# Optimization experiments

Hardware: AMD Instinct MI355X
Metric: run time of the kernel (lower is better)

Reference implementation:

```python
import jax, jax.numpy as jnp
import numpy as np

TOP_K = 10
RANKING_WEIGHT = 0.3
UP_WEIGHT = 1.0
DOWN_WEIGHT = 0.5
NEG = 1e9  # finite stand-in for -inf so softmax/grads stay NaN-free


def setup_inputs() -> dict:
    key = jax.random.key(0)
    k1, k2, k3, k4 = jax.random.split(key, 4)
    B, N = 1024, 5000
    up_logits = jax.random.normal(k1, (B, N), jnp.float32)
    down_logits = jax.random.normal(k2, (B, N), jnp.float32)
    y_true = jax.random.normal(k3, (B, N), jnp.float32) * 0.05  # daily returns
    masks = jax.random.randint(k4, (B, N), 0, 2).astype(jnp.int32)
    return {"up_logits": up_logits, "down_logits": down_logits,
            "y_true": y_true, "masks": masks}


def _bce_with_logits(x, z):
    # softplus(x) - x*z  ==  -[z*log(sig(x)) + (1-z)*log(1-sig(x))]
    return jax.nn.softplus(x) - x * z


def reference(up_logits, down_logits, y_true, masks):
    maskb = masks > 0                                   # [B, N]
    maskf = maskb.astype(up_logits.dtype)
    num_valid = maskf.sum(-1)                           # [B]
    nv_safe = jnp.maximum(num_valid, 1.0)
    k = jnp.minimum(TOP_K, num_valid.astype(jnp.int32))  # [B] min(top_k, num)

    # Descending rank of y_true among valid entries (invalid pushed to bottom).
    y_desc = jnp.where(maskb, y_true, -NEG)
    rank_desc = jnp.argsort(jnp.argsort(-y_desc, axis=-1), axis=-1)  # [B, N]
    up_labels = (rank_desc < k[:, None]).astype(up_logits.dtype)

    # Ascending rank (biggest losers) for down path.
    y_asc = jnp.where(maskb, y_true, NEG)
    rank_asc = jnp.argsort(jnp.argsort(y_asc, axis=-1), axis=-1)
    down_labels = (rank_asc < k[:, None]).astype(down_logits.dtype)

    # Mean BCE over valid entries per row.
    up_loss = jnp.sum(_bce_with_logits(up_logits, up_labels) * maskf, -1) / nv_safe
    down_loss = jnp.sum(_bce_with_logits(down_logits, down_labels) * maskf, -1) / nv_safe

    # Listwise KL: softmax over valid entries; kl_div(log p, q, 'batchmean')
    # with 1D input of size num divides the sum by num.
    logp = jax.nn.log_softmax(jnp.where(maskb, up_logits, -NEG), axis=-1)
    logq = jax.nn.log_softmax(jnp.where(maskb, y_true, -NEG), axis=-1)
    q = jnp.exp(logq)
    kl = jnp.sum(jnp.where(maskb, q * (logq - logp), 0.0), -1) / nv_safe

    batch_loss = UP_WEIGHT * up_loss + DOWN_WEIGHT * down_loss + RANKING_WEIGHT * kl
    batch_loss = jnp.where(num_valid > 0, batch_loss, 0.0)  # skip empty rows
    return jnp.sum(batch_loss) / up_logits.shape[0]
```

## Files before the change

### kernel.cpp

```cpp
#include <hip/hip_runtime.h>
#include <math.h>

#define NCOLS 5000
#define NF4   1250
#define BLOCK 256
#define NITER 5
#define TOPKK 10

__device__ __forceinline__ unsigned mono_f32(float f) {
  unsigned u = __float_as_uint(f);
  return (u & 0x80000000u) ? ~u : (u | 0x80000000u);
}

__device__ __forceinline__ float wave_sum_f(float v) {
#pragma unroll
  for (int o = 1; o < 64; o <<= 1) v += __shfl_xor(v, o);
  return v;
}
__device__ __forceinline__ int wave_sum_i(int v) {
#pragma unroll
  for (int o = 1; o < 64; o <<= 1) v += __shfl_xor(v, o);
  return v;
}
__device__ __forceinline__ unsigned wave_max_u(unsigned v) {
#pragma unroll
  for (int o = 1; o < 64; o <<= 1) {
    unsigned w = __shfl_xor(v, o);
    v = w > v ? w : v;
  }
  return v;
}

__device__ __forceinline__ void insert_desc(unsigned* L, unsigned key) {
  if (key > L[TOPKK - 1]) {
    L[TOPKK - 1] = key;
#pragma unroll
    for (int p = TOPKK - 1; p > 0; --p) {
      unsigned a = L[p - 1], b = L[p];
      L[p - 1] = b > a ? b : a;
      L[p]     = b > a ? a : b;
    }
  }
}

extern "C" __global__ __launch_bounds__(BLOCK, 4)
void row_loss_kernel(const float* __restrict__ up, const float* __restrict__ down,
                     const float* __restrict__ yt, const int* __restrict__ masks,
                     float* __restrict__ out, float inv_nrows) {
  __shared__ float red_f[6][4];
  __shared__ int red_i[4];
  __shared__ unsigned swtop[4 * TOPKK];
  __shared__ unsigned swbot[4 * TOPKK];
  __shared__ unsigned s_thr[2];
  __shared__ float red2[2][4];

  const int row = blockIdx.x;
  const int tid = threadIdx.x;
  const int lane = tid & 63;
  const int wv = tid >> 6;
  const long long b4 = (long long)row * NF4;

  const float4* up4 = (const float4*)up + b4;
  const float4* dn4 = (const float4*)down + b4;
  const float4* yt4 = (const float4*)yt + b4;
  const int4*   mk4 = (const int4*)masks + b4;

  float ym[NITER][4], uu[NITER][4], dd[NITER][4];

  int nv_l = 0;
  float sq = 0.f, sp = 0.f, seyy = 0.f, seyu = 0.f, aspu = 0.f, aspd = 0.f;
  unsigned td[TOPKK], ta[TOPKK];
#pragma unroll
  for (int j = 0; j < TOPKK; ++j) { td[j] = 0u; ta[j] = 0u; }

#pragma unroll
  for (int j = 0; j < NITER; ++j) {
    const int f = j * BLOCK + tid;
    const bool inb = (f < NF4);
    float4 y4 = make_float4(0.f, 0.f, 0.f, 0.f);
    float4 u4 = y4, d4 = y4;
    int4 m4 = make_int4(0, 0, 0, 0);
    if (inb) { y4 = yt4[f]; u4 = up4[f]; d4 = dn4[f]; m4 = mk4[f]; }
    const float* yp = (const float*)&y4;
    const float* upp = (const float*)&u4;
    const float* dp = (const float*)&d4;
    const int* mp = (const int*)&m4;
#pragma unroll
    for (int c = 0; c < 4; ++c) {
      const bool valid = mp[c] > 0;
      const float y = yp[c], u = upp[c], d = dp[c];
      ym[j][c] = valid ? y : -1e9f;
      uu[j][c] = u;
      dd[j][c] = d;
      if (valid) {
        nv_l++;
        const float ey = __expf(y);
        sq += ey;
        seyy += ey * y;
        seyu += ey * u;
        sp += __expf(u);
        aspu += fmaxf(u, 0.f) + __logf(1.f + __expf(-fabsf(u)));
        aspd += fmaxf(d, 0.f) + __logf(1.f + __expf(-fabsf(d)));
        const unsigned kd = mono_f32(y);
        insert_desc(td, kd);
        insert_desc(ta, ~kd);
      }
    }
  }

  nv_l = wave_sum_i(nv_l);
  sq = wave_sum_f(sq);
  sp = wave_sum_f(sp);
  seyy = wave_sum_f(seyy);
  seyu = wave_sum_f(seyu);
  aspu = wave_sum_f(aspu);
  aspd = wave_sum_f(aspd);
  if (lane == 0) {
    red_i[wv] = nv_l;
    red_f[0][wv] = sq;  red_f[1][wv] = sp;
    red_f[2][wv] = seyy; red_f[3][wv] = seyu;
    red_f[4][wv] = aspu; red_f[5][wv] = aspd;
  }

#pragma unroll 1
  for (int r = 0; r < TOPKK; ++r) {
    unsigned m = wave_max_u(td[0]);
    if (td[0] == m && m != 0u) {
#pragma unroll
      for (int j = 0; j < TOPKK - 1; ++j) td[j] = td[j + 1];
      td[TOPKK - 1] = 0u;
    }
    if (lane == 0) swtop[wv * TOPKK + r] = m;
  }
#pragma unroll 1
  for (int r = 0; r < TOPKK; ++r) {
    unsigned m = wave_max_u(ta[0]);
    if (ta[0] == m && m != 0u) {
#pragma unroll
      for (int j = 0; j < TOPKK - 1; ++j) ta[j] = ta[j + 1];
      ta[TOPKK - 1] = 0u;
    }
    if (lane == 0) swbot[wv * TOPKK + r] = m;
  }
  __syncthreads();

  const int nv = red_i[0] + red_i[1] + red_i[2] + red_i[3];
  const int k = nv < TOPKK ? nv : TOPKK;

  if (wv == 0) {
    unsigned v = (lane < 4 * TOPKK) ? swtop[lane] : 0u;
    unsigned thr = 0xFFFFFFFFu;
#pragma unroll 1
    for (int r = 0; r < TOPKK; ++r) {
      unsigned m = wave_max_u(v);
      if (v == m) v = 0u;
      if (r == k - 1) thr = m;
    }
    if (lane == 0) s_thr[0] = thr;
  } else if (wv == 1) {
    unsigned v = (lane < 4 * TOPKK) ? swbot[lane] : 0u;
    unsigned thr = 0xFFFFFFFFu;
#pragma unroll 1
    for (int r = 0; r < TOPKK; ++r) {
      unsigned m = wave_max_u(v);
      if (v == m) v = 0u;
      if (r == k - 1) thr = m;
    }
    if (lane == 0) s_thr[1] = thr;
  }
  __syncthreads();

  const unsigned thr_top = s_thr[0];
  const unsigned thr_bot = s_thr[1];

  float su = 0.f, sd = 0.f;
#pragma unroll
  for (int j = 0; j < NITER; ++j) {
#pragma unroll
    for (int c = 0; c < 4; ++c) {
      const float y = ym[j][c];
      if (y > -1e8f) {
        const unsigned mo = mono_f32(y);
        if (mo >= thr_top) su += uu[j][c];
        if (~mo >= thr_bot) sd += dd[j][c];
      }
    }
  }
  su = wave_sum_f(su);
  sd = wave_sum_f(sd);
  if (lane == 0) { red2[0][wv] = su; red2[1][wv] = sd; }
  __syncthreads();

  if (tid == 0 && nv > 0) {
    const float SQ = (red_f[0][0] + red_f[0][1]) + (red_f[0][2] + red_f[0][3]);
    const float SP = (red_f[1][0] + red_f[1][1]) + (red_f[1][2] + red_f[1][3]);
    const float SYY = (red_f[2][0] + red_f[2][1]) + (red_f[2][2] + red_f[2][3]);
    const float SYU = (red_f[3][0] + red_f[3][1]) + (red_f[3][2] + red_f[3][3]);
    const float ASU = (red_f[4][0] + red_f[4][1]) + (red_f[4][2] + red_f[4][3]);
    const float ASD = (red_f[5][0] + red_f[5][1]) + (red_f[5][2] + red_f[5][3]);
    const float SU = (red2[0][0] + red2[0][1]) + (red2[0][2] + red2[0][3]);
    const float SD = (red2[1][0] + red2[1][1]) + (red2[1][2] + red2[1][3]);
    const float kl = (SYY - SYU) / SQ - __logf(SQ) + __logf(SP);
    const float up_loss = ASU - SU;
    const float dn_loss = ASD - SD;
    const float loss = (up_loss + 0.5f * dn_loss + 0.3f * kl) / (float)nv;
    atomicAdd(out, loss * inv_nrows);
  }
}

extern "C" void kernel_launch(void* const* d_in, const int* in_sizes, int n_in,
                              void* d_out, int out_size, void* d_ws, size_t ws_size,
                              hipStream_t stream) {
  const float* up_logits   = (const float*)d_in[0];
  const float* down_logits = (const float*)d_in[1];
  const float* y_true      = (const float*)d_in[2];
  const int*   masks       = (const int*)d_in[3];

  const int nrows = in_sizes[0] / NCOLS;

  hipMemsetAsync(d_out, 0, sizeof(float) * (size_t)out_size, stream);
  row_loss_kernel<<<nrows, BLOCK, 0, stream>>>(up_logits, down_logits, y_true,
                                               masks, (float*)d_out,
                                               1.0f / (float)nrows);
}
```

Before: 126.1 us.

## Replace per-thread top-k insertion with shared-memory radix histogram selection

Replaces the per-thread sorted top-10 lists and wave-level merges with a 256-bin shared histogram on the top byte of each key. Prefix scans over the histogram locate the bin holding the k-th largest and k-th smallest keys, then only keys in those bins are gathered and refined with wave max/min. The block size doubles to 512 threads, all loads are issued before compute, and the register-heavy insertion sorts go away. The cost is shared-memory atomic contention on a histogram that may be skewed, plus more barriers. The gather caps a boundary bin at 64 keys, which could give wrong thresholds if more keys share that top byte.

```diff
diff --git a/kernel.cpp b/kernel.cpp
--- a/kernel.cpp
+++ b/kernel.cpp
@@ -3,8 +3,9 @@
 
 #define NCOLS 5000
 #define NF4   1250
-#define BLOCK 256
-#define NITER 5
+#define BLOCK 512
+#define NWAVES (BLOCK / 64)
+#define NITER 3
 #define TOPKK 10
 
 __device__ __forceinline__ unsigned mono_f32(float f) {
@@ -30,29 +31,27 @@
   }
   return v;
 }
-
-__device__ __forceinline__ void insert_desc(unsigned* L, unsigned key) {
-  if (key > L[TOPKK - 1]) {
-    L[TOPKK - 1] = key;
-#pragma unroll
-    for (int p = TOPKK - 1; p > 0; --p) {
-      unsigned a = L[p - 1], b = L[p];
-      L[p - 1] = b > a ? b : a;
-      L[p]     = b > a ? a : b;
-    }
-  }
+__device__ __forceinline__ unsigned wave_min_u(unsigned v) {
+#pragma unroll
+  for (int o = 1; o < 64; o <<= 1) {
+    unsigned w = __shfl_xor(v, o);
+    v = w < v ? w : v;
+  }
+  return v;
 }
 
 extern "C" __global__ __launch_bounds__(BLOCK, 4)
 void row_loss_kernel(const float* __restrict__ up, const float* __restrict__ down,
                      const float* __restrict__ yt, const int* __restrict__ masks,
                      float* __restrict__ out, float inv_nrows) {
-  __shared__ float red_f[6][4];
-  __shared__ int red_i[4];
-  __shared__ unsigned swtop[4 * TOPKK];
-  __shared__ unsigned swbot[4 * TOPKK];
+  __shared__ unsigned hist[256];
+  __shared__ float red_f[6][NWAVES];
+  __shared__ int red_i[NWAVES];
+  __shared__ unsigned s_sel[4];
   __shared__ unsigned s_thr[2];
-  __shared__ float red2[2][4];
+  __shared__ unsigned keys_t[64], keys_b[64];
+  __shared__ int cnt_t, cnt_b;
+  __shared__ float red2[2][NWAVES];
 
   const int row = blockIdx.x;
   const int tid = threadIdx.x;
@@ -65,26 +64,33 @@
   const float4* yt4 = (const float4*)yt + b4;
   const int4*   mk4 = (const int4*)masks + b4;
 
+  float4 y4[NITER], u4[NITER], d4[NITER];
+  int4 m4[NITER];
+#pragma unroll
+  for (int j = 0; j < NITER; ++j) {
+    const int f = j * BLOCK + tid;
+    if (f < NF4) {
+      y4[j] = yt4[f]; u4[j] = up4[f]; d4[j] = dn4[f]; m4[j] = mk4[f];
+    } else {
+      y4[j] = make_float4(0.f, 0.f, 0.f, 0.f);
+      u4[j] = y4[j]; d4[j] = y4[j];
+      m4[j] = make_int4(0, 0, 0, 0);
+    }
+  }
+
+  if (tid < 256) hist[tid] = 0u;
+  if (tid == 0) { cnt_t = 0; cnt_b = 0; }
+  __syncthreads();
+
   float ym[NITER][4], uu[NITER][4], dd[NITER][4];
-
   int nv_l = 0;
   float sq = 0.f, sp = 0.f, seyy = 0.f, seyu = 0.f, aspu = 0.f, aspd = 0.f;
-  unsigned td[TOPKK], ta[TOPKK];
-#pragma unroll
-  for (int j = 0; j < TOPKK; ++j) { td[j] = 0u; ta[j] = 0u; }
-
-#pragma unroll
-  for (int j = 0; j < NITER; ++j) {
-    const int f = j * BLOCK + tid;
-    const bool inb = (f < NF4);
-    float4 y4 = make_float4(0.f, 0.f, 0.f, 0.f);
-    float4 u4 = y4, d4 = y4;
-    int4 m4 = make_int4(0, 0, 0, 0);
-    if (inb) { y4 = yt4[f]; u4 = up4[f]; d4 = dn4[f]; m4 = mk4[f]; }
-    const float* yp = (const float*)&y4;
-    const float* upp = (const float*)&u4;
-    const float* dp = (const float*)&d4;
-    const int* mp = (const int*)&m4;
+#pragma unroll
+  for (int j = 0; j < NITER; ++j) {
+    const float* yp = (const float*)&y4[j];
+    const float* upp = (const float*)&u4[j];
+    const float* dp = (const float*)&d4[j];
+    const int* mp = (const int*)&m4[j];
 #pragma unroll
     for (int c = 0; c < 4; ++c) {
       const bool valid = mp[c] > 0;
@@ -101,9 +107,7 @@
         sp += __expf(u);
         aspu += fmaxf(u, 0.f) + __logf(1.f + __expf(-fabsf(u)));
         aspd += fmaxf(d, 0.f) + __logf(1.f + __expf(-fabsf(d)));
-        const unsigned kd = mono_f32(y);
-        insert_desc(td, kd);
-        insert_desc(ta, ~kd);
+        atomicAdd(&hist[mono_f32(y) >> 24], 1u);
       }
     }
   }
@@ -121,68 +125,128 @@
     red_f[2][wv] = seyy; red_f[3][wv] = seyu;
     red_f[4][wv] = aspu; red_f[5][wv] = aspd;
   }
-
-#pragma unroll 1
-  for (int r = 0; r < TOPKK; ++r) {
-    unsigned m = wave_max_u(td[0]);
-    if (td[0] == m && m != 0u) {
-#pragma unroll
-      for (int j = 0; j < TOPKK - 1; ++j) td[j] = td[j + 1];
-      td[TOPKK - 1] = 0u;
-    }
-    if (lane == 0) swtop[wv * TOPKK + r] = m;
-  }
-#pragma unroll 1
-  for (int r = 0; r < TOPKK; ++r) {
-    unsigned m = wave_max_u(ta[0]);
-    if (ta[0] == m && m != 0u) {
-#pragma unroll
-      for (int j = 0; j < TOPKK - 1; ++j) ta[j] = ta[j + 1];
-      ta[TOPKK - 1] = 0u;
-    }
-    if (lane == 0) swbot[wv * TOPKK + r] = m;
-  }
-  __syncthreads();
-
-  const int nv = red_i[0] + red_i[1] + red_i[2] + red_i[3];
+  __syncthreads();
+
+  int nv = 0;
+#pragma unroll
+  for (int w = 0; w < NWAVES; ++w) nv += red_i[w];
   const int k = nv < TOPKK ? nv : TOPKK;
 
   if (wv == 0) {
-    unsigned v = (lane < 4 * TOPKK) ? swtop[lane] : 0u;
-    unsigned thr = 0xFFFFFFFFu;
-#pragma unroll 1
-    for (int r = 0; r < TOPKK; ++r) {
-      unsigned m = wave_max_u(v);
-      if (v == m) v = 0u;
-      if (r == k - 1) thr = m;
-    }
-    if (lane == 0) s_thr[0] = thr;
+    unsigned h[4];
+#pragma unroll
+    for (int j = 0; j < 4; ++j) h[j] = hist[4 * lane + j];
+    const unsigned s = h[0] + h[1] + h[2] + h[3];
+    unsigned suf = s;
+#pragma unroll
+    for (int o = 1; o < 64; o <<= 1) {
+      int src = lane + o;
+      unsigned g = __shfl(suf, src < 64 ? src : lane);
+      suf += (src < 64) ? g : 0u;
+    }
+    unsigned long long mb = __ballot(suf >= (unsigned)k);
+    if (mb != 0ULL) {
+      int lstar = 63 - __builtin_clzll(mb);
+      if (lane == lstar) {
+        unsigned cum = suf - s;
+        int bin = -1; unsigned cab = 0;
+#pragma unroll
+        for (int j = 3; j >= 0; --j) {
+          unsigned nc = cum + h[j];
+          if (bin < 0 && nc >= (unsigned)k) { bin = 4 * lane + j; cab = cum; }
+          cum = nc;
+        }
+        s_sel[0] = (unsigned)bin; s_sel[1] = cab;
+      }
+    } else if (lane == 0) { s_sel[0] = 0xFFFFFFFFu; s_sel[1] = 0u; }
   } else if (wv == 1) {
-    unsigned v = (lane < 4 * TOPKK) ? swbot[lane] : 0u;
-    unsigned thr = 0xFFFFFFFFu;
-#pragma unroll 1
-    for (int r = 0; r < TOPKK; ++r) {
-      unsigned m = wave_max_u(v);
-      if (v == m) v = 0u;
-      if (r == k - 1) thr = m;
-    }
-    if (lane == 0) s_thr[1] = thr;
-  }
-  __syncthreads();
-
-  const unsigned thr_top = s_thr[0];
-  const unsigned thr_bot = s_thr[1];
-
-  float su = 0.f, sd = 0.f;
+    unsigned h[4];
+#pragma unroll
+    for (int j = 0; j < 4; ++j) h[j] = hist[4 * lane + j];
+    const unsigned s = h[0] + h[1] + h[2] + h[3];
+    unsigned pre = s;
+#pragma unroll
+    for (int o = 1; o < 64; o <<= 1) {
+      int src = lane - o;
+      unsigned g = __shfl(pre, src >= 0 ? src : lane);
+      pre += (src >= 0) ? g : 0u;
+    }
+    unsigned long long mb = __ballot(pre >= (unsigned)k);
+    if (mb != 0ULL) {
+      int lstar = __ffsll((unsigned long long)mb) - 1;
+      if (lane == lstar) {
+        unsigned cum = pre - s;
+        int bin = -1; unsigned cbb = 0;
+#pragma unroll
+        for (int j = 0; j < 4; ++j) {
+          unsigned nc = cum + h[j];
+          if (bin < 0 && nc >= (unsigned)k) { bin = 4 * lane + j; cbb = cum; }
+          cum = nc;
+        }
+        s_sel[2] = (unsigned)bin; s_sel[3] = cbb;
+      }
+    } else if (lane == 0) { s_sel[2] = 0xFFFFFFFFu; s_sel[3] = 0u; }
+  }
+  __syncthreads();
+
+  const unsigned bin_top = s_sel[0], cnt_above = s_sel[1];
+  const unsigned bin_bot = s_sel[2], cnt_below = s_sel[3];
+
 #pragma unroll
   for (int j = 0; j < NITER; ++j) {
 #pragma unroll
     for (int c = 0; c < 4; ++c) {
       const float y = ym[j][c];
       if (y > -1e8f) {
-        const unsigned mo = mono_f32(y);
-        if (mo >= thr_top) su += uu[j][c];
-        if (~mo >= thr_bot) sd += dd[j][c];
+        const unsigned kd = mono_f32(y);
+        const unsigned hb = kd >> 24;
+        if (hb == bin_top) { int i = atomicAdd(&cnt_t, 1); if (i < 64) keys_t[i] = kd; }
+        if (hb == bin_bot) { int i = atomicAdd(&cnt_b, 1); if (i < 64) keys_b[i] = kd; }
+      }
+    }
+  }
+  __syncthreads();
+
+  if (wv == 0) {
+    const int n = cnt_t < 64 ? cnt_t : 64;
+    unsigned v = (lane < n) ? keys_t[lane] : 0u;
+    const int rneed = k - (int)cnt_above;
+    unsigned thr = 0xFFFFFFFFu;
+#pragma unroll 1
+    for (int r = 0; r < rneed; ++r) {
+      unsigned m = wave_max_u(v);
+      if (v == m) v = 0u;
+      thr = m;
+    }
+    if (lane == 0) s_thr[0] = thr;
+  } else if (wv == 1) {
+    const int n = cnt_b < 64 ? cnt_b : 64;
+    unsigned v = (lane < n) ? keys_b[lane] : 0xFFFFFFFFu;
+    const int rneed = k - (int)cnt_below;
+    unsigned thr = 0u;
+#pragma unroll 1
+    for (int r = 0; r < rneed; ++r) {
+      unsigned m = wave_min_u(v);
+      if (v == m) v = 0xFFFFFFFFu;
+      thr = m;
+    }
+    if (lane == 0) s_thr[1] = thr;
+  }
+  __syncthreads();
+
+  const unsigned thr_top = s_thr[0];
+  const unsigned thr_bot = s_thr[1];
+
+  float su = 0.f, sd = 0.f;
+#pragma unroll
+  for (int j = 0; j < NITER; ++j) {
+#pragma unroll
+    for (int c = 0; c < 4; ++c) {
+      const float y = ym[j][c];
+      if (y > -1e8f) {
+        const unsigned kd = mono_f32(y);
+        if (kd >= thr_top) su += uu[j][c];
+        if (kd <= thr_bot) sd += dd[j][c];
       }
     }
   }
@@ -192,14 +256,15 @@
   __syncthreads();
 
   if (tid == 0 && nv > 0) {
-    const float SQ = (red_f[0][0] + red_f[0][1]) + (red_f[0][2] + red_f[0][3]);
-    const float SP = (red_f[1][0] + red_f[1][1]) + (red_f[1][2] + red_f[1][3]);
-    const float SYY = (red_f[2][0] + red_f[2][1]) + (red_f[2][2] + red_f[2][3]);
-    const float SYU = (red_f[3][0] + red_f[3][1]) + (red_f[3][2] + red_f[3][3]);
-    const float ASU = (red_f[4][0] + red_f[4][1]) + (red_f[4][2] + red_f[4][3]);
-    const float ASD = (red_f[5][0] + red_f[5][1]) + (red_f[5][2] + red_f[5][3]);
-    const float SU = (red2[0][0] + red2[0][1]) + (red2[0][2] + red2[0][3]);
-    const float SD = (red2[1][0] + red2[1][1]) + (red2[1][2] + red2[1][3]);
+    float SQ = 0.f, SP = 0.f, SYY = 0.f, SYU = 0.f, ASU = 0.f, ASD = 0.f;
+    float SU = 0.f, SD = 0.f;
+#pragma unroll
+    for (int w = 0; w < NWAVES; ++w) {
+      SQ += red_f[0][w]; SP += red_f[1][w];
+      SYY += red_f[2][w]; SYU += red_f[3][w];
+      ASU += red_f[4][w]; ASD += red_f[5][w];
+      SU += red2[0][w]; SD += red2[1][w];
+    }
     const float kl = (SYY - SYU) / SQ - __logf(SQ) + __logf(SP);
     const float up_loss = ASU - SU;
     const float dn_loss = ASD - SD;
```

New measurement: 124.5 us. No clear change (-1.3%).

## Replace per-thread top-10 insertion lists with threshold filtering and shared-memory candidate selection

Applied to the files above, without the earlier changes.

Each thread now keeps only its own max key instead of a register-sorted top-10 list. Each wave takes the 10th-largest of those per-thread maxima as a lower bound, and the max of those bounds over waves is the block cutoff. Elements at or above the cutoff are appended to a capped shared-memory candidate buffer via LDS atomics, and one wave per direction selects the top-k from that buffer. The block grows to 512 threads with fewer iterations per thread, which cuts the per-element insertion cost and register pressure. In exchange it adds shared atomics, and the cap of 256 candidates could overflow on adversarial data.

```diff
diff --git a/kernel.cpp b/kernel.cpp
--- a/kernel.cpp
+++ b/kernel.cpp
@@ -3,9 +3,11 @@
 
 #define NCOLS 5000
 #define NF4   1250
-#define BLOCK 256
-#define NITER 5
+#define BLOCK 512
+#define NWAVES (BLOCK / 64)
+#define NITER 3
 #define TOPKK 10
+#define CAP 256
 
 __device__ __forceinline__ unsigned mono_f32(float f) {
   unsigned u = __float_as_uint(f);
@@ -29,69 +31,71 @@
     v = w > v ? w : v;
   }
   return v;
-}
-
-__device__ __forceinline__ void insert_desc(unsigned* L, unsigned key) {
-  if (key > L[TOPKK - 1]) {
-    L[TOPKK - 1] = key;
-#pragma unroll
-    for (int p = TOPKK - 1; p > 0; --p) {
-      unsigned a = L[p - 1], b = L[p];
-      L[p - 1] = b > a ? b : a;
-      L[p]     = b > a ? a : b;
-    }
-  }
 }
 
 extern "C" __global__ __launch_bounds__(BLOCK, 4)
 void row_loss_kernel(const float* __restrict__ up, const float* __restrict__ down,
                      const float* __restrict__ yt, const int* __restrict__ masks,
                      float* __restrict__ out, float inv_nrows) {
-  __shared__ float red_f[6][4];
-  __shared__ int red_i[4];
-  __shared__ unsigned swtop[4 * TOPKK];
-  __shared__ unsigned swbot[4 * TOPKK];
-  __shared__ unsigned s_thr[2];
-  __shared__ float red2[2][4];
-
-  const int row = blockIdx.x;
+  __shared__ float red_f[6][NWAVES];
+  __shared__ int red_i[NWAVES];
+  __shared__ unsigned t1w_t[NWAVES];
+  __shared__ unsigned t1w_b[NWAVES];
+  __shared__ unsigned keys_t[CAP];
+  __shared__ float    vals_t[CAP];
+  __shared__ unsigned keys_b[CAP];
+  __shared__ float    vals_b[CAP];
+  __shared__ int ct, cb;
+  __shared__ float s_res[2];
+
   const int tid = threadIdx.x;
   const int lane = tid & 63;
   const int wv = tid >> 6;
-  const long long b4 = (long long)row * NF4;
+  const long long b4 = (long long)blockIdx.x * NF4;
 
   const float4* up4 = (const float4*)up + b4;
   const float4* dn4 = (const float4*)down + b4;
   const float4* yt4 = (const float4*)yt + b4;
   const int4*   mk4 = (const int4*)masks + b4;
 
-  float ym[NITER][4], uu[NITER][4], dd[NITER][4];
-
+  if (tid == 0) { ct = 0; cb = 0; }
+
+  float4 y4[NITER], u4[NITER], d4[NITER];
+  int4 m4[NITER];
+#pragma unroll
+  for (int j = 0; j < NITER; ++j) {
+    const int f = j * BLOCK + tid;
+    if (f < NF4) {
+      y4[j] = yt4[f]; u4[j] = up4[f]; d4[j] = dn4[f]; m4[j] = mk4[f];
+    } else {
+      y4[j] = make_float4(0.f, 0.f, 0.f, 0.f);
+      u4[j] = y4[j]; d4[j] = y4[j];
+      m4[j] = make_int4(0, 0, 0, 0);
+    }
+  }
+
+  unsigned km[NITER][4];
+  float uu[NITER][4], dd[NITER][4];
   int nv_l = 0;
   float sq = 0.f, sp = 0.f, seyy = 0.f, seyu = 0.f, aspu = 0.f, aspd = 0.f;
-  unsigned td[TOPKK], ta[TOPKK];
-#pragma unroll
-  for (int j = 0; j < TOPKK; ++j) { td[j] = 0u; ta[j] = 0u; }
-
+  unsigned tmax = 0u, tbmax = 0u;
 #pragma unroll
   for (int j = 0; j < NITER; ++j) {
-    const int f = j * BLOCK + tid;
-    const bool inb = (f < NF4);
-    float4 y4 = make_float4(0.f, 0.f, 0.f, 0.f);
-    float4 u4 = y4, d4 = y4;
-    int4 m4 = make_int4(0, 0, 0, 0);
-    if (inb) { y4 = yt4[f]; u4 = up4[f]; d4 = dn4[f]; m4 = mk4[f]; }
-    const float* yp = (const float*)&y4;
-    const float* upp = (const float*)&u4;
-    const float* dp = (const float*)&d4;
-    const int* mp = (const int*)&m4;
+    const float* yp = (const float*)&y4[j];
+    const float* upp = (const float*)&u4[j];
+    const float* dp = (const float*)&d4[j];
+    const int* mp = (const int*)&m4[j];
 #pragma unroll
     for (int c = 0; c < 4; ++c) {
       const bool valid = mp[c] > 0;
       const float y = yp[c], u = upp[c], d = dp[c];
-      ym[j][c] = valid ? y : -1e9f;
       uu[j][c] = u;
       dd[j][c] = d;
+      const unsigned kd = valid ? mono_f32(y) : 0u;
+      km[j][c] = kd;
+      const unsigned kb = valid ? ~kd : 0u;
+      tmax = kd > tmax ? kd : tmax;
+      tbmax = kb > tbmax ? kb : tbmax;
       if (valid) {
         nv_l++;
         const float ey = __expf(y);
@@ -101,9 +105,6 @@
         sp += __expf(u);
         aspu += fmaxf(u, 0.f) + __logf(1.f + __expf(-fabsf(u)));
         aspd += fmaxf(d, 0.f) + __logf(1.f + __expf(-fabsf(d)));
-        const unsigned kd = mono_f32(y);
-        insert_desc(td, kd);
-        insert_desc(ta, ~kd);
       }
     }
   }
@@ -122,84 +123,131 @@
     red_f[4][wv] = aspu; red_f[5][wv] = aspd;
   }
 
-#pragma unroll 1
-  for (int r = 0; r < TOPKK; ++r) {
-    unsigned m = wave_max_u(td[0]);
-    if (td[0] == m && m != 0u) {
-#pragma unroll
-      for (int j = 0; j < TOPKK - 1; ++j) td[j] = td[j + 1];
-      td[TOPKK - 1] = 0u;
-    }
-    if (lane == 0) swtop[wv * TOPKK + r] = m;
-  }
-#pragma unroll 1
-  for (int r = 0; r < TOPKK; ++r) {
-    unsigned m = wave_max_u(ta[0]);
-    if (ta[0] == m && m != 0u) {
-#pragma unroll
-      for (int j = 0; j < TOPKK - 1; ++j) ta[j] = ta[j + 1];
-      ta[TOPKK - 1] = 0u;
-    }
-    if (lane == 0) swbot[wv * TOPKK + r] = m;
-  }
-  __syncthreads();
-
-  const int nv = red_i[0] + red_i[1] + red_i[2] + red_i[3];
-  const int k = nv < TOPKK ? nv : TOPKK;
-
-  if (wv == 0) {
-    unsigned v = (lane < 4 * TOPKK) ? swtop[lane] : 0u;
-    unsigned thr = 0xFFFFFFFFu;
+  {
+    unsigned v = tmax, t1 = 0u;
 #pragma unroll 1
     for (int r = 0; r < TOPKK; ++r) {
       unsigned m = wave_max_u(v);
       if (v == m) v = 0u;
-      if (r == k - 1) thr = m;
-    }
-    if (lane == 0) s_thr[0] = thr;
-  } else if (wv == 1) {
-    unsigned v = (lane < 4 * TOPKK) ? swbot[lane] : 0u;
-    unsigned thr = 0xFFFFFFFFu;
+      t1 = m;
+    }
+    if (lane == 0) t1w_t[wv] = t1;
+  }
+  {
+    unsigned v = tbmax, t1 = 0u;
 #pragma unroll 1
     for (int r = 0; r < TOPKK; ++r) {
       unsigned m = wave_max_u(v);
       if (v == m) v = 0u;
-      if (r == k - 1) thr = m;
-    }
-    if (lane == 0) s_thr[1] = thr;
+      t1 = m;
+    }
+    if (lane == 0) t1w_b[wv] = t1;
   }
   __syncthreads();
 
-  const unsigned thr_top = s_thr[0];
-  const unsigned thr_bot = s_thr[1];
-
-  float su = 0.f, sd = 0.f;
+  int nv = 0;
+#pragma unroll
+  for (int w = 0; w < NWAVES; ++w) nv += red_i[w];
+  const int k = nv < TOPKK ? nv : TOPKK;
+
+  unsigned t1 = 0u, t1b = 0u;
+#pragma unroll
+  for (int w = 0; w < NWAVES; ++w) {
+    t1 = t1w_t[w] > t1 ? t1w_t[w] : t1;
+    t1b = t1w_b[w] > t1b ? t1w_b[w] : t1b;
+  }
+
 #pragma unroll
   for (int j = 0; j < NITER; ++j) {
 #pragma unroll
     for (int c = 0; c < 4; ++c) {
-      const float y = ym[j][c];
-      if (y > -1e8f) {
-        const unsigned mo = mono_f32(y);
-        if (mo >= thr_top) su += uu[j][c];
-        if (~mo >= thr_bot) sd += dd[j][c];
+      const unsigned kd = km[j][c];
+      if (kd != 0u) {
+        if (kd >= t1) {
+          int i = atomicAdd(&ct, 1);
+          if (i < CAP) { keys_t[i] = kd; vals_t[i] = uu[j][c]; }
+        }
+        const unsigned kb = ~kd;
+        if (kb >= t1b) {
+          int i = atomicAdd(&cb, 1);
+          if (i < CAP) { keys_b[i] = kb; vals_b[i] = dd[j][c]; }
+        }
       }
     }
   }
-  su = wave_sum_f(su);
-  sd = wave_sum_f(sd);
-  if (lane == 0) { red2[0][wv] = su; red2[1][wv] = sd; }
   __syncthreads();
 
+  if (wv == 0) {
+    const int n = ct < CAP ? ct : CAP;
+    unsigned kk[4]; float vvv[4];
+#pragma unroll
+    for (int i = 0; i < 4; ++i) {
+      const int idx = i * 64 + lane;
+      kk[i] = (idx < n) ? keys_t[idx] : 0u;
+      vvv[i] = (idx < n) ? vals_t[idx] : 0.f;
+    }
+    unsigned w0 = kk[0], w1 = kk[1], w2 = kk[2], w3 = kk[3];
+    unsigned thr = 0xFFFFFFFFu;
+#pragma unroll 1
+    for (int r = 0; r < k; ++r) {
+      unsigned lm = w0 > w1 ? w0 : w1;
+      unsigned lm2 = w2 > w3 ? w2 : w3;
+      lm = lm > lm2 ? lm : lm2;
+      unsigned m = wave_max_u(lm);
+      if (w0 == m) w0 = 0u;
+      else if (w1 == m) w1 = 0u;
+      else if (w2 == m) w2 = 0u;
+      else if (w3 == m) w3 = 0u;
+      thr = m;
+    }
+    float su = 0.f;
+#pragma unroll
+    for (int i = 0; i < 4; ++i)
+      if (kk[i] >= thr && kk[i] != 0u) su += vvv[i];
+    su = wave_sum_f(su);
+    if (lane == 0) s_res[0] = su;
+  } else if (wv == 1) {
+    const int n = cb < CAP ? cb : CAP;
+    unsigned kk[4]; float vvv[4];
+#pragma unroll
+    for (int i = 0; i < 4; ++i) {
+      const int idx = i * 64 + lane;
+      kk[i] = (idx < n) ? keys_b[idx] : 0u;
+      vvv[i] = (idx < n) ? vals_b[idx] : 0.f;
+    }
+    unsigned w0 = kk[0], w1 = kk[1], w2 = kk[2], w3 = kk[3];
+    unsigned thr = 0xFFFFFFFFu;
+#pragma unroll 1
+    for (int r = 0; r < k; ++r) {
+      unsigned lm = w0 > w1 ? w0 : w1;
+      unsigned lm2 = w2 > w3 ? w2 : w3;
+      lm = lm > lm2 ? lm : lm2;
+      unsigned m = wave_max_u(lm);
+      if (w0 == m) w0 = 0u;
+      else if (w1 == m) w1 = 0u;
+      else if (w2 == m) w2 = 0u;
+      else if (w3 == m) w3 = 0u;
+      thr = m;
+    }
+    float sd = 0.f;
+#pragma unroll
+    for (int i = 0; i < 4; ++i)
+      if (kk[i] >= thr && kk[i] != 0u) sd += vvv[i];
+    sd = wave_sum_f(sd);
+    if (lane == 0) s_res[1] = sd;
+  }
+  __syncthreads();
+
   if (tid == 0 && nv > 0) {
-    const float SQ = (red_f[0][0] + red_f[0][1]) + (red_f[0][2] + red_f[0][3]);
-    const float SP = (red_f[1][0] + red_f[1][1]) + (red_f[1][2] + red_f[1][3]);
-    const float SYY = (red_f[2][0] + red_f[2][1]) + (red_f[2][2] + red_f[2][3]);
-    const float SYU = (red_f[3][0] + red_f[3][1]) + (red_f[3][2] + red_f[3][3]);
-    const float ASU = (red_f[4][0] + red_f[4][1]) + (red_f[4][2] + red_f[4][3]);
-    const float ASD = (red_f[5][0] + red_f[5][1]) + (red_f[5][2] + red_f[5][3]);
-    const float SU = (red2[0][0] + red2[0][1]) + (red2[0][2] + red2[0][3]);
-    const float SD = (red2[1][0] + red2[1][1]) + (red2[1][2] + red2[1][3]);
+    float SQ = 0.f, SP = 0.f, SYY = 0.f, SYU = 0.f, ASU = 0.f, ASD = 0.f;
+#pragma unroll
+    for (int w = 0; w < NWAVES; ++w) {
+      SQ += red_f[0][w]; SP += red_f[1][w];
+      SYY += red_f[2][w]; SYU += red_f[3][w];
+      ASU += red_f[4][w]; ASD += red_f[5][w];
+    }
+    const float SU = s_res[0];
+    const float SD = s_res[1];
     const float kl = (SYY - SYU) / SQ - __logf(SQ) + __logf(SP);
     const float up_loss = ASU - SU;
     const float dn_loss = ASD - SD;
```

New measurement: 130.4 us. 1.03x slower.
